# Kernel optimization log

Hardware: AMD Instinct MI355X
Metric: run time of the kernel (lower is better)

## Reference

```python
import jax, jax.numpy as jnp
import numpy as np

N_HEADS = 16
NEG = -1e9


def setup_inputs() -> dict:
    key = jax.random.key(0)
    ks = jax.random.split(key, 6)
    B, S, D = 4, 2048, 2048
    scale = 1.0 / np.sqrt(D)
    x = jax.random.normal(ks[0], (B, S, D), dtype=jnp.float32)
    attention_mask = jax.random.randint(ks[1], (B, S), 0, 2, dtype=jnp.int32)
    w_q = jax.random.normal(ks[2], (D, D), dtype=jnp.float32) * scale
    w_k = jax.random.normal(ks[3], (D, D), dtype=jnp.float32) * scale
    w_v = jax.random.normal(ks[4], (D, D), dtype=jnp.float32) * scale
    w_o = jax.random.normal(ks[5], (D, D), dtype=jnp.float32) * scale
    return {"x": x, "attention_mask": attention_mask,
            "w_q": w_q, "w_k": w_k, "w_v": w_v, "w_o": w_o}


def reference(x, attention_mask, w_q, w_k, w_v, w_o):
    B, S, D = x.shape
    H = N_HEADS
    dk = D // H

    def split_heads(t):  # [B,S,D] -> [B,H,S,dk]
        return t.reshape(B, S, H, dk).transpose(0, 2, 1, 3)

    # torch nn.Linear: y = x @ W.T (no bias)
    q = split_heads(x @ w_q.T)
    k = split_heads(x @ w_k.T)
    v = split_heads(x @ w_v.T)

    scores = jnp.einsum('bhqd,bhkd->bhqk', q, k) / jnp.sqrt(jnp.float32(dk))
    # padding mask over keys: [B,1,1,S]
    pad = attention_mask[:, None, None, :] != 0
    scores = jnp.where(pad, scores, NEG)
    # causal mask
    causal = jnp.tril(jnp.ones((S, S), dtype=bool))
    scores = jnp.where(causal[None, None, :, :], scores, NEG)

    attn = jax.nn.softmax(scores, axis=-1)
    # dropout p=0.0 -> identity
    out = jnp.einsum('bhqk,bhkd->bhqd', attn, v)
    out = out.transpose(0, 2, 1, 3).reshape(B, S, D)
    return out @ w_o.T
```

## Files before the change

kernel.cpp:

```cpp
#include <hip/hip_runtime.h>

typedef __bf16 bf16;
typedef __bf16 bf16x4 __attribute__((ext_vector_type(4)));
typedef __bf16 bf16x8 __attribute__((ext_vector_type(8)));
typedef float f32x4 __attribute__((ext_vector_type(4)));
typedef float f32x16 __attribute__((ext_vector_type(16)));

#define NEGF (-1e9f)

__device__ __forceinline__ void gload16(const void* g, void* l) {
  __builtin_amdgcn_global_load_lds(
      (__attribute__((address_space(1))) void*)(void*)g,
      (__attribute__((address_space(3))) void*)l, 16, 0, 0);
}

__global__ __launch_bounds__(256)
void prep_kernel(const float* __restrict__ x, const int* __restrict__ mask,
                 const float* __restrict__ wq, const float* __restrict__ wk,
                 const float* __restrict__ wv, const float* __restrict__ wo,
                 bf16* __restrict__ xb, bf16* __restrict__ wqb,
                 bf16* __restrict__ wkb, bf16* __restrict__ wvb,
                 bf16* __restrict__ wob, float* __restrict__ maskadd)
{
  const float QS = 1.44269504f * 0.08838834764f;
  const size_t i = ((size_t)blockIdx.x * 256 + threadIdx.x) * 4;
  if (i < (size_t)16777216) {
    const float4 v = *(const float4*)&x[i];
    bf16x4 o4 = {(bf16)v.x, (bf16)v.y, (bf16)v.z, (bf16)v.w};
    *(bf16x4*)&xb[i] = o4;
  }
  if (i < (size_t)4194304) {
    float4 v = *(const float4*)&wq[i];
    bf16x4 o4 = {(bf16)(v.x * QS), (bf16)(v.y * QS), (bf16)(v.z * QS), (bf16)(v.w * QS)};
    *(bf16x4*)&wqb[i] = o4;
    v = *(const float4*)&wk[i];
    bf16x4 o5 = {(bf16)v.x, (bf16)v.y, (bf16)v.z, (bf16)v.w};
    *(bf16x4*)&wkb[i] = o5;
    v = *(const float4*)&wv[i];
    bf16x4 o6 = {(bf16)v.x, (bf16)v.y, (bf16)v.z, (bf16)v.w};
    *(bf16x4*)&wvb[i] = o6;
    v = *(const float4*)&wo[i];
    bf16x4 o7 = {(bf16)v.x, (bf16)v.y, (bf16)v.z, (bf16)v.w};
    *(bf16x4*)&wob[i] = o7;
  }
  if (i < (size_t)8192) {
    const int4 m4 = *(const int4*)&mask[i];
    float4 o4 = {m4.x ? 0.f : NEGF, m4.y ? 0.f : NEGF,
                 m4.z ? 0.f : NEGF, m4.w ? 0.f : NEGF};
    *(float4*)&maskadd[i] = o4;
  }
}

__device__ __forceinline__ void gemm_core(
    const bf16* __restrict__ A, const bf16* __restrict__ Bt, int K,
    int rowBase, int colBase, bf16* As, bf16* Bs, f32x16 acc[4][2])
{
  const int t = threadIdx.x;
  const int lane = t & 63;
  const int w = t >> 6;
  const int wm = (w >> 1) << 7;
  const int wn = (w & 1) << 6;
  const int l31 = lane & 31;
  const int half = lane >> 5;

  for (int k0 = 0; k0 < K; k0 += 64) {
    __syncthreads();
#pragma unroll
    for (int i = 0; i < 8; ++i) {
      const int c = (i << 8) + t;
      const int row = c >> 3;
      const int col = ((c & 7) ^ (row & 7)) << 3;
      gload16(&A[(rowBase + row) * K + k0 + col], &As[c << 3]);
    }
#pragma unroll
    for (int i = 0; i < 4; ++i) {
      const int c = (i << 8) + t;
      const int row = c >> 3;
      const int col = ((c & 7) ^ (row & 7)) << 3;
      gload16(&Bt[(colBase + row) * K + k0 + col], &Bs[c << 3]);
    }
    __syncthreads();
#pragma unroll
    for (int kk = 0; kk < 4; ++kk) {
      const int gd = (kk << 1) | half;
      bf16x8 a[4], bfr[2];
#pragma unroll
      for (int mi = 0; mi < 4; ++mi) {
        const int row = wm + (mi << 5) + l31;
        a[mi] = *(const bf16x8*)&As[(row << 6) + ((gd ^ (row & 7)) << 3)];
      }
#pragma unroll
      for (int ni = 0; ni < 2; ++ni) {
        const int row = wn + (ni << 5) + l31;
        bfr[ni] = *(const bf16x8*)&Bs[(row << 6) + ((gd ^ (row & 7)) << 3)];
      }
#pragma unroll
      for (int mi = 0; mi < 4; ++mi)
#pragma unroll
        for (int ni = 0; ni < 2; ++ni)
          acc[mi][ni] = __builtin_amdgcn_mfma_f32_32x32x16_bf16(
              a[mi], bfr[ni], acc[mi][ni], 0, 0, 0);
    }
  }
}

__global__ __launch_bounds__(256, 2)
void qkv_gemm_kernel(const bf16* __restrict__ xb,
                     const bf16* __restrict__ wqb, const bf16* __restrict__ wkb,
                     const bf16* __restrict__ wvb,
                     bf16* __restrict__ qb, bf16* __restrict__ kb,
                     bf16* __restrict__ vtb)
{
  __shared__ __align__(16) bf16 As[256 * 64];
  __shared__ __align__(16) bf16 Bs[128 * 64];
  const int z = blockIdx.z;
  const bf16* Bt = (z == 0) ? wqb : (z == 1) ? wkb : wvb;
  bf16* dst = (z == 0) ? qb : (z == 1) ? kb : vtb;
  const int rowBase = blockIdx.y << 8;
  const int colBase = blockIdx.x << 7;
  f32x16 acc[4][2];
#pragma unroll
  for (int mi = 0; mi < 4; ++mi)
#pragma unroll
    for (int ni = 0; ni < 2; ++ni)
#pragma unroll
      for (int e = 0; e < 16; ++e) acc[mi][ni][e] = 0.f;

  gemm_core(xb, Bt, 2048, rowBase, colBase, As, Bs, acc);

  const int lane = threadIdx.x & 63;
  const int w = threadIdx.x >> 6;
  const int wm = (w >> 1) << 7;
  const int wn = (w & 1) << 6;
  const int l31 = lane & 31;
  const int half = lane >> 5;
#pragma unroll
  for (int mi = 0; mi < 4; ++mi)
#pragma unroll
    for (int ni = 0; ni < 2; ++ni)
#pragma unroll
      for (int r = 0; r < 16; ++r) {
        const int row = rowBase + wm + (mi << 5) + (r & 3) + ((r >> 2) << 3) + (half << 2);
        const int col = colBase + wn + (ni << 5) + l31;
        const int b = row >> 11, s = row & 2047;
        const int h = col >> 7, d = col & 127;
        const bf16 v = (bf16)acc[mi][ni][r];
        if (z == 2) dst[((((b << 4) + h) << 7) + d) * 2048 + s] = v;
        else        dst[(((((b << 4) + h) << 11) + s) << 7) + d] = v;
      }
}

__global__ __launch_bounds__(256, 2)
void out_gemm_kernel(const bf16* __restrict__ attnb, const bf16* __restrict__ wob,
                     float* __restrict__ out)
{
  __shared__ __align__(16) bf16 As[256 * 64];
  __shared__ __align__(16) bf16 Bs[128 * 64];
  const int rowBase = blockIdx.y << 8;
  const int colBase = blockIdx.x << 7;
  f32x16 acc[4][2];
#pragma unroll
  for (int mi = 0; mi < 4; ++mi)
#pragma unroll
    for (int ni = 0; ni < 2; ++ni)
#pragma unroll
      for (int e = 0; e < 16; ++e) acc[mi][ni][e] = 0.f;

  gemm_core(attnb, wob, 2048, rowBase, colBase, As, Bs, acc);

  const int lane = threadIdx.x & 63;
  const int w = threadIdx.x >> 6;
  const int wm = (w >> 1) << 7;
  const int wn = (w & 1) << 6;
  const int l31 = lane & 31;
  const int half = lane >> 5;
#pragma unroll
  for (int mi = 0; mi < 4; ++mi)
#pragma unroll
    for (int ni = 0; ni < 2; ++ni)
#pragma unroll
      for (int r = 0; r < 16; ++r) {
        const int row = rowBase + wm + (mi << 5) + (r & 3) + ((r >> 2) << 3) + (half << 2);
        const int col = colBase + wn + (ni << 5) + l31;
        out[((size_t)row << 11) + col] = acc[mi][ni][r];
      }
}

__global__ __launch_bounds__(256, 2)
void flash_kernel(const bf16* __restrict__ qb, const bf16* __restrict__ kb,
                  const bf16* __restrict__ vtb, const float* __restrict__ maskadd,
                  bf16* __restrict__ attnb)
{
  __shared__ __align__(16) bf16 Ks[64 * 128];
  __shared__ __align__(16) bf16 Vs[128 * 64];

  const int qt = 15 - (int)blockIdx.x;
  const int h = blockIdx.y, b = blockIdx.z;
  const int t = threadIdx.x, lane = t & 63, w = t >> 6;
  const int quad = lane >> 4, l15 = lane & 15;
  const int bh = (b << 4) + h;
  const bf16* Qp = qb + (size_t)bh * (2048 * 128);
  const bf16* Kp = kb + (size_t)bh * (2048 * 128);
  const bf16* Vp = vtb + (size_t)bh * (128 * 2048);
  const int qrow0 = (qt << 7) + (w << 5);

  bf16x8 qf[2][4];
#pragma unroll
  for (int mi = 0; mi < 2; ++mi)
#pragma unroll
    for (int kk = 0; kk < 4; ++kk)
      qf[mi][kk] = *(const bf16x8*)&Qp[((qrow0 + (mi << 4) + l15) << 7) + (kk << 5) + (quad << 3)];

  f32x4 o[2][8];
  float lpart[2][4];
#pragma unroll
  for (int mi = 0; mi < 2; ++mi)
#pragma unroll
    for (int r = 0; r < 4; ++r) lpart[mi][r] = 0.f;
#pragma unroll
  for (int mi = 0; mi < 2; ++mi)
#pragma unroll
    for (int dj = 0; dj < 8; ++dj)
#pragma unroll
      for (int r = 0; r < 4; ++r) o[mi][dj][r] = 0.f;

  bf16* Pw = &Ks[w << 11];
  const int nkt = (qt << 1) + 2;
  for (int kt = 0; kt < nkt; ++kt) {
    __syncthreads();
#pragma unroll
    for (int i = 0; i < 4; ++i) {
      const int c = (i << 8) + t;
      const int row = c >> 4;
      const int col = ((c & 15) ^ (row & 15)) << 3;
      gload16(&Kp[(((kt << 6) + row) << 7) + col], &Ks[c << 3]);
    }
#pragma unroll
    for (int i = 0; i < 4; ++i) {
      const int c = (i << 8) + t;
      const int row = c >> 3;
      const int col = ((c & 7) ^ (row & 7)) << 3;
      gload16(&Vp[(row << 11) + (kt << 6) + col], &Vs[c << 3]);
    }
    __syncthreads();

    const bool skip = (kt << 6) > qrow0 + 31;
    f32x4 S[2][4];
    if (!skip) {
#pragma unroll
      for (int mi = 0; mi < 2; ++mi)
#pragma unroll
        for (int nj = 0; nj < 4; ++nj)
#pragma unroll
          for (int r = 0; r < 4; ++r) S[mi][nj][r] = 0.f;
#pragma unroll
      for (int kk = 0; kk < 4; ++kk) {
        bf16x8 kf[4];
#pragma unroll
        for (int nj = 0; nj < 4; ++nj) {
          const int key = (nj << 4) + l15;
          const int gd = (kk << 2) + quad;
          kf[nj] = *(const bf16x8*)&Ks[(key << 7) + ((gd ^ (key & 15)) << 3)];
        }
#pragma unroll
        for (int mi = 0; mi < 2; ++mi)
#pragma unroll
          for (int nj = 0; nj < 4; ++nj)
            S[mi][nj] = __builtin_amdgcn_mfma_f32_16x16x32_bf16(qf[mi][kk], kf[nj], S[mi][nj], 0, 0, 0);
      }
      float mv[4];
#pragma unroll
      for (int nj = 0; nj < 4; ++nj)
        mv[nj] = maskadd[(b << 11) + (kt << 6) + (nj << 4) + l15];
      const bool diag = ((kt << 6) + 63 > qrow0);
#pragma unroll
      for (int mi = 0; mi < 2; ++mi)
#pragma unroll
        for (int nj = 0; nj < 4; ++nj)
#pragma unroll
          for (int r = 0; r < 4; ++r) {
            float s = S[mi][nj][r] + mv[nj];
            if (diag) {
              const int key = (kt << 6) + (nj << 4) + l15;
              const int qrow = qrow0 + (mi << 4) + (quad << 2) + r;
              if (key > qrow) s += NEGF;
            }
            const float p = __builtin_amdgcn_exp2f(s);
            S[mi][nj][r] = p;
            lpart[mi][r] += p;
          }
    }
    __syncthreads();
    if (!skip) {
#pragma unroll
      for (int mi = 0; mi < 2; ++mi)
#pragma unroll
        for (int nj = 0; nj < 4; ++nj)
#pragma unroll
          for (int r = 0; r < 4; ++r) {
            const int row = (mi << 4) + (quad << 2) + r;
            const int col = (nj << 4) + l15;
            Pw[(row << 6) + ((((col >> 3) ^ (row & 7)) << 3) | (col & 7))] = (bf16)S[mi][nj][r];
          }
#pragma unroll
      for (int kk = 0; kk < 2; ++kk) {
        bf16x8 pf[2];
#pragma unroll
        for (int mi = 0; mi < 2; ++mi) {
          const int row = (mi << 4) + l15;
          pf[mi] = *(const bf16x8*)&Pw[(row << 6) + ((((kk << 2) + quad) ^ (row & 7)) << 3)];
        }
#pragma unroll
        for (int dj = 0; dj < 8; ++dj) {
          const int d = (dj << 4) + l15;
          const int gd = (kk << 2) + quad;
          const bf16x8 vf = *(const bf16x8*)&Vs[(d << 6) + ((gd ^ (d & 7)) << 3)];
#pragma unroll
          for (int mi = 0; mi < 2; ++mi)
            o[mi][dj] = __builtin_amdgcn_mfma_f32_16x16x32_bf16(pf[mi], vf, o[mi][dj], 0, 0, 0);
        }
      }
    }
  }

#pragma unroll
  for (int mi = 0; mi < 2; ++mi)
#pragma unroll
    for (int r = 0; r < 4; ++r) {
      float s = lpart[mi][r];
#pragma unroll
      for (int off = 1; off < 16; off <<= 1) s += __shfl_xor(s, off);
      const float inv = 1.0f / s;
      const int row = qrow0 + (mi << 4) + (quad << 2) + r;
#pragma unroll
      for (int dj = 0; dj < 8; ++dj) {
        const int d = (dj << 4) + l15;
        attnb[((size_t)((b << 11) + row) << 11) + (h << 7) + d] = (bf16)(o[mi][dj][r] * inv);
      }
    }
}

__global__ void scan_mask_kernel(const int* __restrict__ mask, int* __restrict__ firstone)
{
  __shared__ int fm;
  for (int b = 0; b < 4; ++b) {
    if (threadIdx.x == 0) fm = 2048;
    __syncthreads();
    int lm = 2048;
    for (int s = threadIdx.x; s < 2048; s += 256)
      if (mask[(b << 11) + s] != 0) lm = min(lm, s);
    atomicMin(&fm, lm);
    __syncthreads();
    if (threadIdx.x == 0) firstone[b] = fm;
    __syncthreads();
  }
}

__global__ void mean_v_kernel(const bf16* __restrict__ vtb, float* __restrict__ meanv)
{
  const int row = blockIdx.x;
  float sum = 0.f;
  for (int s = threadIdx.x; s < 2048; s += 256)
    sum += (float)vtb[((size_t)row << 11) + s];
#pragma unroll
  for (int off = 1; off < 64; off <<= 1) sum += __shfl_xor(sum, off);
  __shared__ float part[4];
  if ((threadIdx.x & 63) == 0) part[threadIdx.x >> 6] = sum;
  __syncthreads();
  if (threadIdx.x == 0)
    meanv[row] = (part[0] + part[1] + part[2] + part[3]) * (1.0f / 2048.0f);
}

__global__ void fixup_kernel(const int* __restrict__ firstone,
                             const float* __restrict__ meanv,
                             bf16* __restrict__ attnb)
{
  const int b = blockIdx.x, h = blockIdx.y, d = threadIdx.x;
  const int f = firstone[b];
  const bf16 v = (bf16)meanv[(((b << 4) + h) << 7) + d];
  for (int s = 0; s < f; ++s)
    attnb[((size_t)((b << 11) + s) << 11) + (h << 7) + d] = v;
}

extern "C" void kernel_launch(void* const* d_in, const int* in_sizes, int n_in,
                              void* d_out, int out_size, void* d_ws, size_t ws_size,
                              hipStream_t stream)
{
  const float* x  = (const float*)d_in[0];
  const int* mask = (const int*)d_in[1];
  const float* wq = (const float*)d_in[2];
  const float* wk = (const float*)d_in[3];
  const float* wv = (const float*)d_in[4];
  const float* wo = (const float*)d_in[5];
  float* out = (float*)d_out;

  char* ws = (char*)d_ws;
  bf16* xb      = (bf16*)(ws + 0);
  bf16* wqb     = (bf16*)(ws + 33554432);
  bf16* wkb     = (bf16*)(ws + 41943040);
  bf16* wvb     = (bf16*)(ws + 50331648);
  bf16* wob     = (bf16*)(ws + 58720256);
  bf16* qb      = (bf16*)(ws + 67108864);
  bf16* kb      = (bf16*)(ws + 100663296);
  bf16* vtb     = (bf16*)(ws + 134217728);
  bf16* attnb   = (bf16*)(ws + 167772160);
  float* maskadd= (float*)(ws + 201326592);
  float* meanv  = (float*)(ws + 201359360);
  int* firstone = (int*)(ws + 201392128);

  prep_kernel<<<16384, 256, 0, stream>>>(x, mask, wq, wk, wv, wo,
                                         xb, wqb, wkb, wvb, wob, maskadd);
  qkv_gemm_kernel<<<dim3(16, 32, 3), 256, 0, stream>>>(xb, wqb, wkb, wvb, qb, kb, vtb);
  scan_mask_kernel<<<1, 256, 0, stream>>>(mask, firstone);
  mean_v_kernel<<<8192, 256, 0, stream>>>(vtb, meanv);
  flash_kernel<<<dim3(16, 16, 4), 256, 0, stream>>>(qb, kb, vtb, maskadd, attnb);
  fixup_kernel<<<dim3(4, 16), 128, 0, stream>>>(firstone, meanv, attnb);
  out_gemm_kernel<<<dim3(16, 32), 256, 0, stream>>>(attnb, wob, out);
}
```

Before: 689.9 us.

## Shrink GEMM tiles to 128x128 with 16x16 MFMA and fold mask scan into prep

The QKV and output projection GEMMs move from 256x128 block tiles with 32x32x16 MFMA to 128x128 tiles with 16x16x32 MFMA. This doubles the grid so more workgroups are in flight, and it cuts LDS use per block. In exchange, each tile reuses loaded data less, so more global traffic is needed per unit of compute. The single-block scan_mask kernel is merged into the last block of prep_kernel, removing one kernel launch.

```diff
diff --git a/kernel.cpp b/kernel.cpp
--- a/kernel.cpp
+++ b/kernel.cpp
@@ -4,7 +4,6 @@
 typedef __bf16 bf16x4 __attribute__((ext_vector_type(4)));
 typedef __bf16 bf16x8 __attribute__((ext_vector_type(8)));
 typedef float f32x4 __attribute__((ext_vector_type(4)));
-typedef float f32x16 __attribute__((ext_vector_type(16)));
 
 #define NEGF (-1e9f)
 
@@ -20,7 +19,8 @@
                  const float* __restrict__ wv, const float* __restrict__ wo,
                  bf16* __restrict__ xb, bf16* __restrict__ wqb,
                  bf16* __restrict__ wkb, bf16* __restrict__ wvb,
-                 bf16* __restrict__ wob, float* __restrict__ maskadd)
+                 bf16* __restrict__ wob, float* __restrict__ maskadd,
+                 int* __restrict__ firstone)
 {
   const float QS = 1.44269504f * 0.08838834764f;
   const size_t i = ((size_t)blockIdx.x * 256 + threadIdx.x) * 4;
@@ -49,57 +49,70 @@
                  m4.z ? 0.f : NEGF, m4.w ? 0.f : NEGF};
     *(float4*)&maskadd[i] = o4;
   }
-}
-
-__device__ __forceinline__ void gemm_core(
+  if (blockIdx.x == 16383) {
+    __shared__ int fm;
+    for (int b = 0; b < 4; ++b) {
+      if (threadIdx.x == 0) fm = 2048;
+      __syncthreads();
+      int lm = 2048;
+      for (int s = threadIdx.x; s < 2048; s += 256)
+        if (mask[(b << 11) + s] != 0) lm = min(lm, s);
+      atomicMin(&fm, lm);
+      __syncthreads();
+      if (threadIdx.x == 0) firstone[b] = fm;
+      __syncthreads();
+    }
+  }
+}
+
+__device__ __forceinline__ void gemm_core128(
     const bf16* __restrict__ A, const bf16* __restrict__ Bt, int K,
-    int rowBase, int colBase, bf16* As, bf16* Bs, f32x16 acc[4][2])
+    int rowBase, int colBase, bf16* As, bf16* Bs, f32x4 acc[4][4])
 {
   const int t = threadIdx.x;
   const int lane = t & 63;
   const int w = t >> 6;
-  const int wm = (w >> 1) << 7;
+  const int wm = (w >> 1) << 6;
   const int wn = (w & 1) << 6;
-  const int l31 = lane & 31;
-  const int half = lane >> 5;
+  const int l15 = lane & 15;
+  const int quad = lane >> 4;
 
   for (int k0 = 0; k0 < K; k0 += 64) {
     __syncthreads();
-#pragma unroll
-    for (int i = 0; i < 8; ++i) {
-      const int c = (i << 8) + t;
-      const int row = c >> 3;
-      const int col = ((c & 7) ^ (row & 7)) << 3;
-      gload16(&A[(rowBase + row) * K + k0 + col], &As[c << 3]);
-    }
 #pragma unroll
     for (int i = 0; i < 4; ++i) {
       const int c = (i << 8) + t;
       const int row = c >> 3;
       const int col = ((c & 7) ^ (row & 7)) << 3;
-      gload16(&Bt[(colBase + row) * K + k0 + col], &Bs[c << 3]);
+      gload16(&A[(size_t)(rowBase + row) * K + k0 + col], &As[c << 3]);
+    }
+#pragma unroll
+    for (int i = 0; i < 4; ++i) {
+      const int c = (i << 8) + t;
+      const int row = c >> 3;
+      const int col = ((c & 7) ^ (row & 7)) << 3;
+      gload16(&Bt[(size_t)(colBase + row) * K + k0 + col], &Bs[c << 3]);
     }
     __syncthreads();
 #pragma unroll
-    for (int kk = 0; kk < 4; ++kk) {
-      const int gd = (kk << 1) | half;
-      bf16x8 a[4], bfr[2];
+    for (int ks = 0; ks < 2; ++ks) {
+      bf16x8 a[4], b[4];
 #pragma unroll
       for (int mi = 0; mi < 4; ++mi) {
-        const int row = wm + (mi << 5) + l31;
-        a[mi] = *(const bf16x8*)&As[(row << 6) + ((gd ^ (row & 7)) << 3)];
-      }
-#pragma unroll
-      for (int ni = 0; ni < 2; ++ni) {
-        const int row = wn + (ni << 5) + l31;
-        bfr[ni] = *(const bf16x8*)&Bs[(row << 6) + ((gd ^ (row & 7)) << 3)];
+        const int row = wm + (mi << 4) + l15;
+        a[mi] = *(const bf16x8*)&As[(row << 6) + ((((ks << 2) + quad) ^ (row & 7)) << 3)];
+      }
+#pragma unroll
+      for (int ni = 0; ni < 4; ++ni) {
+        const int row = wn + (ni << 4) + l15;
+        b[ni] = *(const bf16x8*)&Bs[(row << 6) + ((((ks << 2) + quad) ^ (row & 7)) << 3)];
       }
 #pragma unroll
       for (int mi = 0; mi < 4; ++mi)
 #pragma unroll
-        for (int ni = 0; ni < 2; ++ni)
-          acc[mi][ni] = __builtin_amdgcn_mfma_f32_32x32x16_bf16(
-              a[mi], bfr[ni], acc[mi][ni], 0, 0, 0);
+        for (int ni = 0; ni < 4; ++ni)
+          acc[mi][ni] = __builtin_amdgcn_mfma_f32_16x16x32_bf16(
+              a[mi], b[ni], acc[mi][ni], 0, 0, 0);
     }
   }
 }
@@ -111,37 +124,37 @@
                      bf16* __restrict__ qb, bf16* __restrict__ kb,
                      bf16* __restrict__ vtb)
 {
-  __shared__ __align__(16) bf16 As[256 * 64];
+  __shared__ __align__(16) bf16 As[128 * 64];
   __shared__ __align__(16) bf16 Bs[128 * 64];
   const int z = blockIdx.z;
   const bf16* Bt = (z == 0) ? wqb : (z == 1) ? wkb : wvb;
   bf16* dst = (z == 0) ? qb : (z == 1) ? kb : vtb;
-  const int rowBase = blockIdx.y << 8;
+  const int rowBase = blockIdx.y << 7;
   const int colBase = blockIdx.x << 7;
-  f32x16 acc[4][2];
+  f32x4 acc[4][4];
 #pragma unroll
   for (int mi = 0; mi < 4; ++mi)
 #pragma unroll
-    for (int ni = 0; ni < 2; ++ni)
-#pragma unroll
-      for (int e = 0; e < 16; ++e) acc[mi][ni][e] = 0.f;
-
-  gemm_core(xb, Bt, 2048, rowBase, colBase, As, Bs, acc);
+    for (int ni = 0; ni < 4; ++ni)
+#pragma unroll
+      for (int r = 0; r < 4; ++r) acc[mi][ni][r] = 0.f;
+
+  gemm_core128(xb, Bt, 2048, rowBase, colBase, As, Bs, acc);
 
   const int lane = threadIdx.x & 63;
   const int w = threadIdx.x >> 6;
-  const int wm = (w >> 1) << 7;
+  const int wm = (w >> 1) << 6;
   const int wn = (w & 1) << 6;
-  const int l31 = lane & 31;
-  const int half = lane >> 5;
+  const int l15 = lane & 15;
+  const int quad = lane >> 4;
 #pragma unroll
   for (int mi = 0; mi < 4; ++mi)
 #pragma unroll
-    for (int ni = 0; ni < 2; ++ni)
-#pragma unroll
-      for (int r = 0; r < 16; ++r) {
-        const int row = rowBase + wm + (mi << 5) + (r & 3) + ((r >> 2) << 3) + (half << 2);
-        const int col = colBase + wn + (ni << 5) + l31;
+    for (int ni = 0; ni < 4; ++ni)
+#pragma unroll
+      for (int r = 0; r < 4; ++r) {
+        const int row = rowBase + wm + (mi << 4) + (quad << 2) + r;
+        const int col = colBase + wn + (ni << 4) + l15;
         const int b = row >> 11, s = row & 2047;
         const int h = col >> 7, d = col & 127;
         const bf16 v = (bf16)acc[mi][ni][r];
@@ -154,34 +167,34 @@
 void out_gemm_kernel(const bf16* __restrict__ attnb, const bf16* __restrict__ wob,
                      float* __restrict__ out)
 {
-  __shared__ __align__(16) bf16 As[256 * 64];
+  __shared__ __align__(16) bf16 As[128 * 64];
   __shared__ __align__(16) bf16 Bs[128 * 64];
-  const int rowBase = blockIdx.y << 8;
+  const int rowBase = blockIdx.y << 7;
   const int colBase = blockIdx.x << 7;
-  f32x16 acc[4][2];
+  f32x4 acc[4][4];
 #pragma unroll
   for (int mi = 0; mi < 4; ++mi)
 #pragma unroll
-    for (int ni = 0; ni < 2; ++ni)
-#pragma unroll
-      for (int e = 0; e < 16; ++e) acc[mi][ni][e] = 0.f;
-
-  gemm_core(attnb, wob, 2048, rowBase, colBase, As, Bs, acc);
+    for (int ni = 0; ni < 4; ++ni)
+#pragma unroll
+      for (int r = 0; r < 4; ++r) acc[mi][ni][r] = 0.f;
+
+  gemm_core128(attnb, wob, 2048, rowBase, colBase, As, Bs, acc);
 
   const int lane = threadIdx.x & 63;
   const int w = threadIdx.x >> 6;
-  const int wm = (w >> 1) << 7;
+  const int wm = (w >> 1) << 6;
   const int wn = (w & 1) << 6;
-  const int l31 = lane & 31;
-  const int half = lane >> 5;
+  const int l15 = lane & 15;
+  const int quad = lane >> 4;
 #pragma unroll
   for (int mi = 0; mi < 4; ++mi)
 #pragma unroll
-    for (int ni = 0; ni < 2; ++ni)
-#pragma unroll
-      for (int r = 0; r < 16; ++r) {
-        const int row = rowBase + wm + (mi << 5) + (r & 3) + ((r >> 2) << 3) + (half << 2);
-        const int col = colBase + wn + (ni << 5) + l31;
+    for (int ni = 0; ni < 4; ++ni)
+#pragma unroll
+      for (int r = 0; r < 4; ++r) {
+        const int row = rowBase + wm + (mi << 4) + (quad << 2) + r;
+        const int col = colBase + wn + (ni << 4) + l15;
         out[((size_t)row << 11) + col] = acc[mi][ni][r];
       }
 }
@@ -338,22 +351,6 @@
         attnb[((size_t)((b << 11) + row) << 11) + (h << 7) + d] = (bf16)(o[mi][dj][r] * inv);
       }
     }
-}
-
-__global__ void scan_mask_kernel(const int* __restrict__ mask, int* __restrict__ firstone)
-{
-  __shared__ int fm;
-  for (int b = 0; b < 4; ++b) {
-    if (threadIdx.x == 0) fm = 2048;
-    __syncthreads();
-    int lm = 2048;
-    for (int s = threadIdx.x; s < 2048; s += 256)
-      if (mask[(b << 11) + s] != 0) lm = min(lm, s);
-    atomicMin(&fm, lm);
-    __syncthreads();
-    if (threadIdx.x == 0) firstone[b] = fm;
-    __syncthreads();
-  }
 }
 
 __global__ void mean_v_kernel(const bf16* __restrict__ vtb, float* __restrict__ meanv)
@@ -409,11 +406,10 @@
   int* firstone = (int*)(ws + 201392128);
 
   prep_kernel<<<16384, 256, 0, stream>>>(x, mask, wq, wk, wv, wo,
-                                         xb, wqb, wkb, wvb, wob, maskadd);
-  qkv_gemm_kernel<<<dim3(16, 32, 3), 256, 0, stream>>>(xb, wqb, wkb, wvb, qb, kb, vtb);
-  scan_mask_kernel<<<1, 256, 0, stream>>>(mask, firstone);
+                                         xb, wqb, wkb, wvb, wob, maskadd, firstone);
+  qkv_gemm_kernel<<<dim3(16, 64, 3), 256, 0, stream>>>(xb, wqb, wkb, wvb, qb, kb, vtb);
   mean_v_kernel<<<8192, 256, 0, stream>>>(vtb, meanv);
   flash_kernel<<<dim3(16, 16, 4), 256, 0, stream>>>(qb, kb, vtb, maskadd, attnb);
   fixup_kernel<<<dim3(4, 16), 128, 0, stream>>>(firstone, meanv, attnb);
-  out_gemm_kernel<<<dim3(16, 32), 256, 0, stream>>>(attnb, wob, out);
-}
+  out_gemm_kernel<<<dim3(16, 64), 256, 0, stream>>>(attnb, wob, out);
+}
```

New measurement: 658.9 us. 4.5% less time.
